# Kernel optimization log

Hardware: AMD Instinct MI355X
Metric: run time of the kernel (lower is better)

The kernel has to match this reference:

```python
import jax, jax.numpy as jnp
import numpy as np

B, L, D = 4096, 200, 64
N_ITEMS, N_USERS, N_RATINGS = 100000, 100000, 5


def setup_inputs() -> dict:
    key = jax.random.key(0)
    ks = jax.random.split(key, 10)
    nodes = jax.random.randint(ks[0], (B,), 0, N_USERS)
    history_uv = jax.random.randint(ks[1], (B, L), 0, N_ITEMS)
    history_r = jax.random.randint(ks[2], (B, L), 0, N_RATINGS)
    s = 1.0 / np.sqrt(D)
    v2e = jax.random.normal(ks[3], (N_ITEMS, D), dtype=jnp.float32)
    r2e = jax.random.normal(ks[4], (N_RATINGS, D), dtype=jnp.float32)
    # torch Linear: weight is [out, in]
    w1_W = jax.random.uniform(ks[5], (D, 2 * D), dtype=jnp.float32, minval=-s, maxval=s)
    w1_b = jax.random.uniform(ks[6], (D,), dtype=jnp.float32, minval=-s, maxval=s)
    w2_W = jax.random.uniform(ks[7], (D, D), dtype=jnp.float32, minval=-s, maxval=s)
    w2_b = jax.random.uniform(ks[8], (D,), dtype=jnp.float32, minval=-s, maxval=s)
    return {
        "v2e": v2e, "r2e": r2e,
        "w1_W": w1_W, "w1_b": w1_b, "w2_W": w2_W, "w2_b": w2_b,
        "nodes": nodes, "history_uv": history_uv, "history_r": history_r,
    }


def reference(v2e, r2e, w1_W, w1_b, w2_W, w2_b, nodes, history_uv, history_r):
    # Gather item and rating embeddings for every (node, history slot): [B, L, D]
    e_uv = v2e[history_uv]
    e_r = r2e[history_r]
    # concat -> [B, L, 2D], two-layer MLP with ReLU
    x = jnp.concatenate([e_uv, e_r], axis=-1)
    h = jax.nn.relu(jnp.einsum("bli,oi->blo", x, w1_W) + w1_b)
    o = jax.nn.relu(jnp.einsum("bli,oi->blo", h, w2_W) + w2_b)
    # uv=True branch: plain mean over the history dimension (nodes/u2e unused)
    return jnp.mean(o, axis=1)  # [B, D]
```

## Files before the change

kernel.cpp:

```cpp
#include <hip/hip_runtime.h>

#define NITEMS 100000
#define NRATE  5
#define BB     4096
#define LL     200
#define DD     64
#define NBUV   391

typedef short short8  __attribute__((ext_vector_type(8)));
typedef short short4v __attribute__((ext_vector_type(4)));
typedef float f32x4   __attribute__((ext_vector_type(4)));

static __device__ __forceinline__ short f2bf(float f) {
  unsigned u = __builtin_bit_cast(unsigned, f);
  u += 0x7fffu + ((u >> 16) & 1u);
  return (short)(u >> 16);
}
static __device__ __forceinline__ float bf2f(short s) {
  return __builtin_bit_cast(float, (unsigned)((unsigned short)s) << 16);
}
static __device__ __forceinline__ int kperm(int p) {
  return ((p & 3) << 4) | (p >> 2);
}

__global__ __launch_bounds__(256) void k_pre(
    const float* __restrict__ v2e, const float* __restrict__ r2e,
    const float* __restrict__ w1W, const float* __restrict__ w1b,
    const float* __restrict__ w2W,
    short* __restrict__ pre_uv, short* __restrict__ w2p,
    float* __restrict__ r5p)
{
  const int tid = threadIdx.x;
  const int blk = blockIdx.x;

  if (blk >= NBUV) {
    for (int idx = tid; idx < 64 * 64; idx += 256) {
      const int o = idx >> 6, p = idx & 63;
      w2p[idx] = f2bf(w2W[o * 64 + kperm(p)]);
    }
    for (int idx = tid; idx < NRATE * 64; idx += 256) {
      const int r = idx >> 6, p = idx & 63;
      const int o = kperm(p);
      const float4* wr = reinterpret_cast<const float4*>(w1W + o * 128 + 64);
      const float4* rr = reinterpret_cast<const float4*>(r2e + r * 64);
      float s = w1b[o];
#pragma unroll
      for (int q = 0; q < 16; ++q) {
        const float4 a = wr[q], b = rr[q];
        s += a.x * b.x + a.y * b.y + a.z * b.z + a.w * b.w;
      }
      r5p[r * 64 + p] = s;
    }
    return;
  }

  const int wave = tid >> 6, lane = tid & 63;
  const int n = lane & 15, quad = lane >> 4;

  short8 bfr[2][4];
#pragma unroll
  for (int nt = 0; nt < 4; ++nt)
#pragma unroll
    for (int kh = 0; kh < 2; ++kh) {
      const float4* p = reinterpret_cast<const float4*>(
          w1W + (nt * 16 + n) * 128 + kh * 32 + quad * 8);
      const float4 x0 = p[0], x1 = p[1];
      short8 f;
      f[0] = f2bf(x0.x); f[1] = f2bf(x0.y); f[2] = f2bf(x0.z); f[3] = f2bf(x0.w);
      f[4] = f2bf(x1.x); f[5] = f2bf(x1.y); f[6] = f2bf(x1.z); f[7] = f2bf(x1.w);
      bfr[kh][nt] = f;
    }

  const int ibase_w = blk * 256 + wave * 64;

  float4 cur0, cur1, cur2, cur3;
  {
    const int row = min(ibase_w + n, NITEMS - 1);
    const float4* p = reinterpret_cast<const float4*>(v2e + (size_t)row * 64 + quad * 8);
    cur0 = p[0]; cur1 = p[1];
    const float4* q = reinterpret_cast<const float4*>(v2e + (size_t)row * 64 + 32 + quad * 8);
    cur2 = q[0]; cur3 = q[1];
  }

#pragma unroll
  for (int it = 0; it < 4; ++it) {
    float4 nx0, nx1, nx2, nx3;
    if (it < 3) {
      const int row = min(ibase_w + (it + 1) * 16 + n, NITEMS - 1);
      const float4* p = reinterpret_cast<const float4*>(v2e + (size_t)row * 64 + quad * 8);
      nx0 = p[0]; nx1 = p[1];
      const float4* q = reinterpret_cast<const float4*>(v2e + (size_t)row * 64 + 32 + quad * 8);
      nx2 = q[0]; nx3 = q[1];
    }

    short8 afr[2];
    {
      short8 a;
      a[0] = f2bf(cur0.x); a[1] = f2bf(cur0.y); a[2] = f2bf(cur0.z); a[3] = f2bf(cur0.w);
      a[4] = f2bf(cur1.x); a[5] = f2bf(cur1.y); a[6] = f2bf(cur1.z); a[7] = f2bf(cur1.w);
      afr[0] = a;
      a[0] = f2bf(cur2.x); a[1] = f2bf(cur2.y); a[2] = f2bf(cur2.z); a[3] = f2bf(cur2.w);
      a[4] = f2bf(cur3.x); a[5] = f2bf(cur3.y); a[6] = f2bf(cur3.z); a[7] = f2bf(cur3.w);
      afr[1] = a;
    }

    f32x4 d[4];
#pragma unroll
    for (int nt = 0; nt < 4; ++nt) {
      f32x4 z = {0.f, 0.f, 0.f, 0.f};
      z = __builtin_amdgcn_mfma_f32_16x16x32_bf16(afr[0], bfr[0][nt], z, 0, 0, 0);
      z = __builtin_amdgcn_mfma_f32_16x16x32_bf16(afr[1], bfr[1][nt], z, 0, 0, 0);
      d[nt] = z;
    }

#pragma unroll
    for (int r = 0; r < 4; ++r) {
      const int item = ibase_w + it * 16 + quad * 4 + r;
      if (item < NITEMS) {
        short4v s = {f2bf(d[0][r]), f2bf(d[1][r]), f2bf(d[2][r]), f2bf(d[3][r])};
        *reinterpret_cast<short4v*>(pre_uv + (size_t)item * 64 + n * 4) = s;
      }
    }

    if (it < 3) { cur0 = nx0; cur1 = nx1; cur2 = nx2; cur3 = nx3; }
  }
}

__global__ __launch_bounds__(256) void k_main(
    const short* __restrict__ pre_uv, const float* __restrict__ r5p,
    const short* __restrict__ w2p, const float* __restrict__ w2b,
    const int* __restrict__ huv, const int* __restrict__ hrr,
    float* __restrict__ out)
{
  __shared__ __align__(16) float s_r5[5 * 68];
  __shared__ float red[4][64];

  const int tid  = threadIdx.x;
  const int wave = tid >> 6, lane = tid & 63;
  const int n = lane & 15, quad = lane >> 4;
  const int b = blockIdx.x;
  const int ntiles = (wave == 0) ? 4 : 3;

  for (int idx = tid; idx < 5 * 64; idx += 256)
    s_r5[(idx >> 6) * 68 + (idx & 63)] = r5p[idx];

  const int* hu = huv + b * LL;
  const int* hr = hrr + b * LL;
  int iv[4] = {0, 0, 0, 0}, ir[4] = {0, 0, 0, 0};
#pragma unroll
  for (int t = 0; t < 4; ++t)
    if (t < ntiles) {
      const int lc = min(wave * 16 + t * 64 + n, LL - 1);
      iv[t] = hu[lc];
      ir[t] = hr[lc];
    }

  short8 bfr[2][4];
#pragma unroll
  for (int nt = 0; nt < 4; ++nt)
#pragma unroll
    for (int kh = 0; kh < 2; ++kh)
      bfr[kh][nt] = *reinterpret_cast<const short8*>(
          w2p + (nt * 16 + n) * 64 + kh * 32 + quad * 8);

  float bias[4];
#pragma unroll
  for (int nt = 0; nt < 4; ++nt) bias[nt] = w2b[nt * 16 + n];

  short8 u[4][2];
#pragma unroll
  for (int t = 0; t < 4; ++t)
    if (t < ntiles)
#pragma unroll
      for (int kh = 0; kh < 2; ++kh)
        u[t][kh] = *reinterpret_cast<const short8*>(
            pre_uv + (size_t)iv[t] * 64 + kh * 32 + quad * 8);

  __syncthreads();

  float acc[4] = {0.f, 0.f, 0.f, 0.f};
#pragma unroll
  for (int t = 0; t < 4; ++t) {
    if (t >= ntiles) continue;
    short8 afr[2];
#pragma unroll
    for (int kh = 0; kh < 2; ++kh) {
      const float4* rp = reinterpret_cast<const float4*>(
          s_r5 + ir[t] * 68 + kh * 32 + quad * 8);
      const float4 r0 = rp[0], r1 = rp[1];
      const float rv[8] = {r0.x, r0.y, r0.z, r0.w, r1.x, r1.y, r1.z, r1.w};
      short8 a;
#pragma unroll
      for (int j = 0; j < 8; ++j) {
        const float h = bf2f(u[t][kh][j]) + rv[j];
        a[j] = f2bf(fmaxf(h, 0.f));
      }
      afr[kh] = a;
    }

    f32x4 d[4];
#pragma unroll
    for (int nt = 0; nt < 4; ++nt) {
      f32x4 z = {0.f, 0.f, 0.f, 0.f};
      z = __builtin_amdgcn_mfma_f32_16x16x32_bf16(afr[0], bfr[0][nt], z, 0, 0, 0);
      z = __builtin_amdgcn_mfma_f32_16x16x32_bf16(afr[1], bfr[1][nt], z, 0, 0, 0);
      d[nt] = z;
    }

    const int lbase = wave * 16 + t * 64;
#pragma unroll
    for (int nt = 0; nt < 4; ++nt)
#pragma unroll
      for (int r = 0; r < 4; ++r) {
        const int rl = lbase + quad * 4 + r;
        const float v = fmaxf(d[nt][r] + bias[nt], 0.f);
        acc[nt] += (rl < LL) ? v : 0.f;
      }
  }

#pragma unroll
  for (int nt = 0; nt < 4; ++nt) {
    float v = acc[nt];
    v += __shfl_xor(v, 16, 64);
    v += __shfl_xor(v, 32, 64);
    acc[nt] = v;
  }

  if (lane < 16) {
#pragma unroll
    for (int nt = 0; nt < 4; ++nt) red[wave][nt * 16 + lane] = acc[nt];
  }
  __syncthreads();
  if (tid < 64) {
    const float s = red[0][tid] + red[1][tid] + red[2][tid] + red[3][tid];
    out[b * 64 + tid] = s * (1.0f / (float)LL);
  }
}

__global__ __launch_bounds__(256) void k_fallback(
    const float* __restrict__ v2e, const float* __restrict__ r2e,
    const float* __restrict__ w1W, const float* __restrict__ w1b,
    const float* __restrict__ w2W, const float* __restrict__ w2b,
    const int* __restrict__ huv, const int* __restrict__ hrr,
    float* __restrict__ out)
{
  __shared__ float sw1[64][129];
  __shared__ float sw2[64][65];
  __shared__ float sx[4][128];
  __shared__ float sh[4][64];
  __shared__ float red[4][64];

  const int tid = threadIdx.x;
  const int wave = tid >> 6, lane = tid & 63;
  const int b = blockIdx.x;

  for (int idx = tid; idx < 64 * 128; idx += 256) sw1[idx >> 7][idx & 127] = w1W[idx];
  for (int idx = tid; idx < 64 * 64; idx += 256) sw2[idx >> 6][idx & 63] = w2W[idx];
  __syncthreads();

  const float b1o = w1b[lane], b2o = w2b[lane];
  float acc = 0.f;

  for (int l = wave; l < LL; l += 4) {
    const int iv = huv[b * LL + l];
    const int ir = hrr[b * LL + l];
    sx[wave][lane]      = v2e[iv * 64 + lane];
    sx[wave][64 + lane] = r2e[ir * 64 + lane];
    __syncthreads();
    float h = b1o;
    for (int i = 0; i < 128; ++i) h += sx[wave][i] * sw1[lane][i];
    sh[wave][lane] = fmaxf(h, 0.f);
    __syncthreads();
    float o = b2o;
    for (int i = 0; i < 64; ++i) o += sh[wave][i] * sw2[lane][i];
    acc += fmaxf(o, 0.f);
  }

  red[wave][lane] = acc;
  __syncthreads();
  if (tid < 64) {
    const float s = red[0][tid] + red[1][tid] + red[2][tid] + red[3][tid];
    out[b * 64 + tid] = s * (1.0f / (float)LL);
  }
}

extern "C" void kernel_launch(void* const* d_in, const int* in_sizes, int n_in,
                              void* d_out, int out_size, void* d_ws, size_t ws_size,
                              hipStream_t stream) {
  (void)in_sizes; (void)n_in; (void)out_size;
  const float* v2e = (const float*)d_in[0];
  const float* r2e = (const float*)d_in[1];
  const float* w1W = (const float*)d_in[2];
  const float* w1b = (const float*)d_in[3];
  const float* w2W = (const float*)d_in[4];
  const float* w2b = (const float*)d_in[5];
  const int* huv = (const int*)d_in[7];
  const int* hrr = (const int*)d_in[8];
  float* out = (float*)d_out;

  const size_t OFF_R5 = (size_t)NITEMS * 64 * sizeof(short);
  const size_t OFF_W2 = OFF_R5 + NRATE * 64 * sizeof(float);
  const size_t NEED   = OFF_W2 + 64 * 64 * sizeof(short);

  if (ws_size >= NEED) {
    short* pre_uv = (short*)d_ws;
    float* r5p    = (float*)((char*)d_ws + OFF_R5);
    short* w2p    = (short*)((char*)d_ws + OFF_W2);

    k_pre<<<NBUV + 1, 256, 0, stream>>>(v2e, r2e, w1W, w1b, w2W, pre_uv, w2p, r5p);
    k_main<<<BB, 256, 0, stream>>>(pre_uv, r5p, w2p, w2b, huv, hrr, out);
  } else {
    k_fallback<<<BB, 256, 0, stream>>>(v2e, r2e, w1W, w1b, w2W, w2b, huv, hrr, out);
  }
}
```

Baseline: 125.0 us.

## Split item precompute across more blocks and vectorize bf16 packing in both kernels

The item-projection kernel now launches four times as many blocks, each wave handling a single 16-item tile instead of looping over four with software prefetch. This aims for more parallelism and memory-level concurrency. bf16 conversion now packs two values with a perm instruction. The main kernel unrolls three full tiles, peels the tail tile for wave 0 with a mask, and uses packed float2 arithmetic for the bias, ReLU and accumulation. The tradeoff is less per-wave latency hiding in the precompute and more code size in the main kernel.

```diff
diff --git a/kernel.cpp b/kernel.cpp
--- a/kernel.cpp
+++ b/kernel.cpp
@@ -5,19 +5,24 @@
 #define BB     4096
 #define LL     200
 #define DD     64
-#define NBUV   391
+#define NBUV   1563
 
 typedef short short8  __attribute__((ext_vector_type(8)));
 typedef short short4v __attribute__((ext_vector_type(4)));
 typedef float f32x4   __attribute__((ext_vector_type(4)));
-
+typedef float f32x2   __attribute__((ext_vector_type(2)));
+typedef int   i32x4   __attribute__((ext_vector_type(4)));
+typedef int   i32x2   __attribute__((ext_vector_type(2)));
+
+static __device__ __forceinline__ unsigned rtne16(float f) {
+  unsigned u = __builtin_bit_cast(unsigned, f);
+  return u + 0x7fffu + ((u >> 16) & 1u);
+}
+static __device__ __forceinline__ unsigned pk2bf(float a, float b) {
+  return __builtin_amdgcn_perm(rtne16(b), rtne16(a), 0x07060302u);
+}
 static __device__ __forceinline__ short f2bf(float f) {
-  unsigned u = __builtin_bit_cast(unsigned, f);
-  u += 0x7fffu + ((u >> 16) & 1u);
-  return (short)(u >> 16);
-}
-static __device__ __forceinline__ float bf2f(short s) {
-  return __builtin_bit_cast(float, (unsigned)((unsigned short)s) << 16);
+  return (short)(rtne16(f) >> 16);
 }
 static __device__ __forceinline__ int kperm(int p) {
   return ((p & 3) << 4) | (p >> 2);
@@ -56,6 +61,7 @@
 
   const int wave = tid >> 6, lane = tid & 63;
   const int n = lane & 15, quad = lane >> 4;
+  const int ibase = blk * 64 + wave * 16;
 
   short8 bfr[2][4];
 #pragma unroll
@@ -65,64 +71,39 @@
       const float4* p = reinterpret_cast<const float4*>(
           w1W + (nt * 16 + n) * 128 + kh * 32 + quad * 8);
       const float4 x0 = p[0], x1 = p[1];
-      short8 f;
-      f[0] = f2bf(x0.x); f[1] = f2bf(x0.y); f[2] = f2bf(x0.z); f[3] = f2bf(x0.w);
-      f[4] = f2bf(x1.x); f[5] = f2bf(x1.y); f[6] = f2bf(x1.z); f[7] = f2bf(x1.w);
-      bfr[kh][nt] = f;
-    }
-
-  const int ibase_w = blk * 256 + wave * 64;
-
-  float4 cur0, cur1, cur2, cur3;
-  {
-    const int row = min(ibase_w + n, NITEMS - 1);
-    const float4* p = reinterpret_cast<const float4*>(v2e + (size_t)row * 64 + quad * 8);
-    cur0 = p[0]; cur1 = p[1];
-    const float4* q = reinterpret_cast<const float4*>(v2e + (size_t)row * 64 + 32 + quad * 8);
-    cur2 = q[0]; cur3 = q[1];
-  }
-
-#pragma unroll
-  for (int it = 0; it < 4; ++it) {
-    float4 nx0, nx1, nx2, nx3;
-    if (it < 3) {
-      const int row = min(ibase_w + (it + 1) * 16 + n, NITEMS - 1);
-      const float4* p = reinterpret_cast<const float4*>(v2e + (size_t)row * 64 + quad * 8);
-      nx0 = p[0]; nx1 = p[1];
-      const float4* q = reinterpret_cast<const float4*>(v2e + (size_t)row * 64 + 32 + quad * 8);
-      nx2 = q[0]; nx3 = q[1];
-    }
-
-    short8 afr[2];
-    {
-      short8 a;
-      a[0] = f2bf(cur0.x); a[1] = f2bf(cur0.y); a[2] = f2bf(cur0.z); a[3] = f2bf(cur0.w);
-      a[4] = f2bf(cur1.x); a[5] = f2bf(cur1.y); a[6] = f2bf(cur1.z); a[7] = f2bf(cur1.w);
-      afr[0] = a;
-      a[0] = f2bf(cur2.x); a[1] = f2bf(cur2.y); a[2] = f2bf(cur2.z); a[3] = f2bf(cur2.w);
-      a[4] = f2bf(cur3.x); a[5] = f2bf(cur3.y); a[6] = f2bf(cur3.z); a[7] = f2bf(cur3.w);
-      afr[1] = a;
-    }
-
-    f32x4 d[4];
-#pragma unroll
-    for (int nt = 0; nt < 4; ++nt) {
-      f32x4 z = {0.f, 0.f, 0.f, 0.f};
-      z = __builtin_amdgcn_mfma_f32_16x16x32_bf16(afr[0], bfr[0][nt], z, 0, 0, 0);
-      z = __builtin_amdgcn_mfma_f32_16x16x32_bf16(afr[1], bfr[1][nt], z, 0, 0, 0);
-      d[nt] = z;
-    }
-
-#pragma unroll
-    for (int r = 0; r < 4; ++r) {
-      const int item = ibase_w + it * 16 + quad * 4 + r;
-      if (item < NITEMS) {
-        short4v s = {f2bf(d[0][r]), f2bf(d[1][r]), f2bf(d[2][r]), f2bf(d[3][r])};
-        *reinterpret_cast<short4v*>(pre_uv + (size_t)item * 64 + n * 4) = s;
-      }
-    }
-
-    if (it < 3) { cur0 = nx0; cur1 = nx1; cur2 = nx2; cur3 = nx3; }
+      i32x4 pk = {(int)pk2bf(x0.x, x0.y), (int)pk2bf(x0.z, x0.w),
+                  (int)pk2bf(x1.x, x1.y), (int)pk2bf(x1.z, x1.w)};
+      bfr[kh][nt] = __builtin_bit_cast(short8, pk);
+    }
+
+  const int arow = min(ibase + n, NITEMS - 1);
+  short8 afr[2];
+#pragma unroll
+  for (int kh = 0; kh < 2; ++kh) {
+    const float4* p = reinterpret_cast<const float4*>(
+        v2e + (size_t)arow * 64 + kh * 32 + quad * 8);
+    const float4 x0 = p[0], x1 = p[1];
+    i32x4 pk = {(int)pk2bf(x0.x, x0.y), (int)pk2bf(x0.z, x0.w),
+                (int)pk2bf(x1.x, x1.y), (int)pk2bf(x1.z, x1.w)};
+    afr[kh] = __builtin_bit_cast(short8, pk);
+  }
+
+  f32x4 d[4];
+#pragma unroll
+  for (int nt = 0; nt < 4; ++nt) {
+    f32x4 z = {0.f, 0.f, 0.f, 0.f};
+    z = __builtin_amdgcn_mfma_f32_16x16x32_bf16(afr[0], bfr[0][nt], z, 0, 0, 0);
+    z = __builtin_amdgcn_mfma_f32_16x16x32_bf16(afr[1], bfr[1][nt], z, 0, 0, 0);
+    d[nt] = z;
+  }
+
+#pragma unroll
+  for (int r = 0; r < 4; ++r) {
+    const int item = ibase + quad * 4 + r;
+    if (item < NITEMS) {
+      i32x2 s = {(int)pk2bf(d[0][r], d[1][r]), (int)pk2bf(d[2][r], d[3][r])};
+      *reinterpret_cast<i32x2*>(pre_uv + (size_t)item * 64 + n * 4) = s;
+    }
   }
 }
 
@@ -139,21 +120,25 @@
   const int wave = tid >> 6, lane = tid & 63;
   const int n = lane & 15, quad = lane >> 4;
   const int b = blockIdx.x;
-  const int ntiles = (wave == 0) ? 4 : 3;
 
   for (int idx = tid; idx < 5 * 64; idx += 256)
     s_r5[(idx >> 6) * 68 + (idx & 63)] = r5p[idx];
 
   const int* hu = huv + b * LL;
   const int* hr = hrr + b * LL;
-  int iv[4] = {0, 0, 0, 0}, ir[4] = {0, 0, 0, 0};
-#pragma unroll
-  for (int t = 0; t < 4; ++t)
-    if (t < ntiles) {
-      const int lc = min(wave * 16 + t * 64 + n, LL - 1);
-      iv[t] = hu[lc];
-      ir[t] = hr[lc];
-    }
+  int iv[4], ir[4];
+#pragma unroll
+  for (int t = 0; t < 3; ++t) {
+    const int lc = wave * 16 + t * 64 + n;
+    iv[t] = hu[lc];
+    ir[t] = hr[lc];
+  }
+  const bool has_tail = (wave == 0);
+  if (has_tail) {
+    const int lc = min(192 + n, LL - 1);
+    iv[3] = hu[lc];
+    ir[3] = hr[lc];
+  }
 
   short8 bfr[2][4];
 #pragma unroll
@@ -163,39 +148,48 @@
       bfr[kh][nt] = *reinterpret_cast<const short8*>(
           w2p + (nt * 16 + n) * 64 + kh * 32 + quad * 8);
 
-  float bias[4];
-#pragma unroll
-  for (int nt = 0; nt < 4; ++nt) bias[nt] = w2b[nt * 16 + n];
+  f32x2 bias2[4];
+#pragma unroll
+  for (int nt = 0; nt < 4; ++nt) {
+    const float bv = w2b[nt * 16 + n];
+    bias2[nt] = f32x2{bv, bv};
+  }
 
   short8 u[4][2];
 #pragma unroll
-  for (int t = 0; t < 4; ++t)
-    if (t < ntiles)
-#pragma unroll
-      for (int kh = 0; kh < 2; ++kh)
-        u[t][kh] = *reinterpret_cast<const short8*>(
-            pre_uv + (size_t)iv[t] * 64 + kh * 32 + quad * 8);
+  for (int t = 0; t < 3; ++t)
+#pragma unroll
+    for (int kh = 0; kh < 2; ++kh)
+      u[t][kh] = *reinterpret_cast<const short8*>(
+          pre_uv + (size_t)iv[t] * 64 + kh * 32 + quad * 8);
+  if (has_tail)
+#pragma unroll
+    for (int kh = 0; kh < 2; ++kh)
+      u[3][kh] = *reinterpret_cast<const short8*>(
+          pre_uv + (size_t)iv[3] * 64 + kh * 32 + quad * 8);
 
   __syncthreads();
 
-  float acc[4] = {0.f, 0.f, 0.f, 0.f};
-#pragma unroll
-  for (int t = 0; t < 4; ++t) {
-    if (t >= ntiles) continue;
+  f32x2 acc2[4] = {{0.f, 0.f}, {0.f, 0.f}, {0.f, 0.f}, {0.f, 0.f}};
+
+#pragma unroll
+  for (int t = 0; t < 3; ++t) {
     short8 afr[2];
 #pragma unroll
     for (int kh = 0; kh < 2; ++kh) {
-      const float4* rp = reinterpret_cast<const float4*>(
+      const i32x4 up = __builtin_bit_cast(i32x4, u[t][kh]);
+      const f32x2* rp = reinterpret_cast<const f32x2*>(
           s_r5 + ir[t] * 68 + kh * 32 + quad * 8);
-      const float4 r0 = rp[0], r1 = rp[1];
-      const float rv[8] = {r0.x, r0.y, r0.z, r0.w, r1.x, r1.y, r1.z, r1.w};
-      short8 a;
-#pragma unroll
-      for (int j = 0; j < 8; ++j) {
-        const float h = bf2f(u[t][kh][j]) + rv[j];
-        a[j] = f2bf(fmaxf(h, 0.f));
+      i32x4 hpk;
+#pragma unroll
+      for (int j = 0; j < 4; ++j) {
+        const unsigned p = (unsigned)up[j];
+        f32x2 uf = {__builtin_bit_cast(float, p << 16),
+                    __builtin_bit_cast(float, p & 0xffff0000u)};
+        f32x2 s = uf + rp[j];
+        hpk[j] = (int)pk2bf(fmaxf(s.x, 0.f), fmaxf(s.y, 0.f));
       }
-      afr[kh] = a;
+      afr[kh] = __builtin_bit_cast(short8, hpk);
     }
 
     f32x4 d[4];
@@ -207,20 +201,61 @@
       d[nt] = z;
     }
 
-    const int lbase = wave * 16 + t * 64;
-#pragma unroll
-    for (int nt = 0; nt < 4; ++nt)
-#pragma unroll
-      for (int r = 0; r < 4; ++r) {
-        const int rl = lbase + quad * 4 + r;
-        const float v = fmaxf(d[nt][r] + bias[nt], 0.f);
-        acc[nt] += (rl < LL) ? v : 0.f;
+#pragma unroll
+    for (int nt = 0; nt < 4; ++nt) {
+      f32x2 p0 = f32x2{d[nt][0], d[nt][1]} + bias2[nt];
+      f32x2 p1 = f32x2{d[nt][2], d[nt][3]} + bias2[nt];
+      p0.x = fmaxf(p0.x, 0.f); p0.y = fmaxf(p0.y, 0.f);
+      p1.x = fmaxf(p1.x, 0.f); p1.y = fmaxf(p1.y, 0.f);
+      acc2[nt] += p0 + p1;
+    }
+  }
+
+  if (has_tail) {
+    const float m = (quad < 2) ? 1.0f : 0.0f;
+    short8 afr[2];
+#pragma unroll
+    for (int kh = 0; kh < 2; ++kh) {
+      const i32x4 up = __builtin_bit_cast(i32x4, u[3][kh]);
+      const f32x2* rp = reinterpret_cast<const f32x2*>(
+          s_r5 + ir[3] * 68 + kh * 32 + quad * 8);
+      i32x4 hpk;
+#pragma unroll
+      for (int j = 0; j < 4; ++j) {
+        const unsigned p = (unsigned)up[j];
+        f32x2 uf = {__builtin_bit_cast(float, p << 16),
+                    __builtin_bit_cast(float, p & 0xffff0000u)};
+        f32x2 s = uf + rp[j];
+        hpk[j] = (int)pk2bf(fmaxf(s.x, 0.f), fmaxf(s.y, 0.f));
       }
-  }
-
+      afr[kh] = __builtin_bit_cast(short8, hpk);
+    }
+
+    f32x4 d[4];
+#pragma unroll
+    for (int nt = 0; nt < 4; ++nt) {
+      f32x4 z = {0.f, 0.f, 0.f, 0.f};
+      z = __builtin_amdgcn_mfma_f32_16x16x32_bf16(afr[0], bfr[0][nt], z, 0, 0, 0);
+      z = __builtin_amdgcn_mfma_f32_16x16x32_bf16(afr[1], bfr[1][nt], z, 0, 0, 0);
+      d[nt] = z;
+    }
+
+#pragma unroll
+    for (int nt = 0; nt < 4; ++nt) {
+      f32x2 p0 = f32x2{d[nt][0], d[nt][1]} + bias2[nt];
+      f32x2 p1 = f32x2{d[nt][2], d[nt][3]} + bias2[nt];
+      p0.x = fmaxf(p0.x, 0.f); p0.y = fmaxf(p0.y, 0.f);
+      p1.x = fmaxf(p1.x, 0.f); p1.y = fmaxf(p1.y, 0.f);
+      const f32x2 s = p0 + p1;
+      acc2[nt].x += s.x * m;
+      acc2[nt].y += s.y * m;
+    }
+  }
+
+  float acc[4];
 #pragma unroll
   for (int nt = 0; nt < 4; ++nt) {
-    float v = acc[nt];
+    float v = acc2[nt].x + acc2[nt].y;
     v += __shfl_xor(v, 16, 64);
     v += __shfl_xor(v, 32, 64);
     acc[nt] = v;
```

New measurement: 134.5 us. +7.6%, slower.

## Assign one wavefront per batch row and pack bf16 conversions

Applied to the files above, without the earlier changes.

k_main now gives each wave a whole batch row, processing 13 history tiles per wave instead of splitting 200 slots over four waves. This removes the shared-memory cross-wave reduction and the second barrier, and issues all 26 embedding gathers up front. The fp32-to-bf16 conversion switches from round-to-nearest-even to a cheaper round-half-up, packed pairwise with v_perm. The layer-1 add/ReLU and bias/accumulate steps use float2 vector math. In exchange, register pressure rises from holding 13 tiles of gathered data, and the rounding behaviour changes slightly.

```diff
diff --git a/kernel.cpp b/kernel.cpp
--- a/kernel.cpp
+++ b/kernel.cpp
@@ -8,16 +8,18 @@
 #define NBUV   391
 
 typedef short short8  __attribute__((ext_vector_type(8)));
-typedef short short4v __attribute__((ext_vector_type(4)));
 typedef float f32x4   __attribute__((ext_vector_type(4)));
+typedef float f32x2   __attribute__((ext_vector_type(2)));
+typedef int   i32x4   __attribute__((ext_vector_type(4)));
+typedef int   i32x2   __attribute__((ext_vector_type(2)));
 
 static __device__ __forceinline__ short f2bf(float f) {
-  unsigned u = __builtin_bit_cast(unsigned, f);
-  u += 0x7fffu + ((u >> 16) & 1u);
-  return (short)(u >> 16);
-}
-static __device__ __forceinline__ float bf2f(short s) {
-  return __builtin_bit_cast(float, (unsigned)((unsigned short)s) << 16);
+  return (short)((__builtin_bit_cast(unsigned, f) + 0x8000u) >> 16);
+}
+static __device__ __forceinline__ unsigned pk2bf(float a, float b) {
+  const unsigned ua = __builtin_bit_cast(unsigned, a) + 0x8000u;
+  const unsigned ub = __builtin_bit_cast(unsigned, b) + 0x8000u;
+  return __builtin_amdgcn_perm(ub, ua, 0x07060302u);
 }
 static __device__ __forceinline__ int kperm(int p) {
   return ((p & 3) << 4) | (p >> 2);
@@ -65,10 +67,9 @@
       const float4* p = reinterpret_cast<const float4*>(
           w1W + (nt * 16 + n) * 128 + kh * 32 + quad * 8);
       const float4 x0 = p[0], x1 = p[1];
-      short8 f;
-      f[0] = f2bf(x0.x); f[1] = f2bf(x0.y); f[2] = f2bf(x0.z); f[3] = f2bf(x0.w);
-      f[4] = f2bf(x1.x); f[5] = f2bf(x1.y); f[6] = f2bf(x1.z); f[7] = f2bf(x1.w);
-      bfr[kh][nt] = f;
+      i32x4 pk = {(int)pk2bf(x0.x, x0.y), (int)pk2bf(x0.z, x0.w),
+                  (int)pk2bf(x1.x, x1.y), (int)pk2bf(x1.z, x1.w)};
+      bfr[kh][nt] = __builtin_bit_cast(short8, pk);
     }
 
   const int ibase_w = blk * 256 + wave * 64;
@@ -95,13 +96,12 @@
 
     short8 afr[2];
     {
-      short8 a;
-      a[0] = f2bf(cur0.x); a[1] = f2bf(cur0.y); a[2] = f2bf(cur0.z); a[3] = f2bf(cur0.w);
-      a[4] = f2bf(cur1.x); a[5] = f2bf(cur1.y); a[6] = f2bf(cur1.z); a[7] = f2bf(cur1.w);
-      afr[0] = a;
-      a[0] = f2bf(cur2.x); a[1] = f2bf(cur2.y); a[2] = f2bf(cur2.z); a[3] = f2bf(cur2.w);
-      a[4] = f2bf(cur3.x); a[5] = f2bf(cur3.y); a[6] = f2bf(cur3.z); a[7] = f2bf(cur3.w);
-      afr[1] = a;
+      i32x4 pk0 = {(int)pk2bf(cur0.x, cur0.y), (int)pk2bf(cur0.z, cur0.w),
+                   (int)pk2bf(cur1.x, cur1.y), (int)pk2bf(cur1.z, cur1.w)};
+      afr[0] = __builtin_bit_cast(short8, pk0);
+      i32x4 pk1 = {(int)pk2bf(cur2.x, cur2.y), (int)pk2bf(cur2.z, cur2.w),
+                   (int)pk2bf(cur3.x, cur3.y), (int)pk2bf(cur3.z, cur3.w)};
+      afr[1] = __builtin_bit_cast(short8, pk1);
     }
 
     f32x4 d[4];
@@ -117,8 +117,8 @@
     for (int r = 0; r < 4; ++r) {
       const int item = ibase_w + it * 16 + quad * 4 + r;
       if (item < NITEMS) {
-        short4v s = {f2bf(d[0][r]), f2bf(d[1][r]), f2bf(d[2][r]), f2bf(d[3][r])};
-        *reinterpret_cast<short4v*>(pre_uv + (size_t)item * 64 + n * 4) = s;
+        i32x2 s = {(int)pk2bf(d[0][r], d[1][r]), (int)pk2bf(d[2][r], d[3][r])};
+        *reinterpret_cast<i32x2*>(pre_uv + (size_t)item * 64 + n * 4) = s;
       }
     }
 
@@ -133,27 +133,37 @@
     float* __restrict__ out)
 {
   __shared__ __align__(16) float s_r5[5 * 68];
-  __shared__ float red[4][64];
 
   const int tid  = threadIdx.x;
   const int wave = tid >> 6, lane = tid & 63;
   const int n = lane & 15, quad = lane >> 4;
-  const int b = blockIdx.x;
-  const int ntiles = (wave == 0) ? 4 : 3;
+  const int b = blockIdx.x * 4 + wave;
 
   for (int idx = tid; idx < 5 * 64; idx += 256)
     s_r5[(idx >> 6) * 68 + (idx & 63)] = r5p[idx];
 
   const int* hu = huv + b * LL;
   const int* hr = hrr + b * LL;
-  int iv[4] = {0, 0, 0, 0}, ir[4] = {0, 0, 0, 0};
-#pragma unroll
-  for (int t = 0; t < 4; ++t)
-    if (t < ntiles) {
-      const int lc = min(wave * 16 + t * 64 + n, LL - 1);
-      iv[t] = hu[lc];
-      ir[t] = hr[lc];
-    }
+
+  int iv[13], ir[13];
+#pragma unroll
+  for (int t = 0; t < 12; ++t) {
+    iv[t] = hu[t * 16 + n];
+    ir[t] = hr[t * 16 + n];
+  }
+  {
+    const int lc = min(192 + n, LL - 1);
+    iv[12] = hu[lc];
+    ir[12] = hr[lc];
+  }
+
+  short8 u[13][2];
+#pragma unroll
+  for (int t = 0; t < 13; ++t)
+#pragma unroll
+    for (int kh = 0; kh < 2; ++kh)
+      u[t][kh] = *reinterpret_cast<const short8*>(
+          pre_uv + (size_t)iv[t] * 64 + kh * 32 + quad * 8);
 
   short8 bfr[2][4];
 #pragma unroll
@@ -163,39 +173,36 @@
       bfr[kh][nt] = *reinterpret_cast<const short8*>(
           w2p + (nt * 16 + n) * 64 + kh * 32 + quad * 8);
 
-  float bias[4];
-#pragma unroll
-  for (int nt = 0; nt < 4; ++nt) bias[nt] = w2b[nt * 16 + n];
-
-  short8 u[4][2];
-#pragma unroll
-  for (int t = 0; t < 4; ++t)
-    if (t < ntiles)
-#pragma unroll
-      for (int kh = 0; kh < 2; ++kh)
-        u[t][kh] = *reinterpret_cast<const short8*>(
-            pre_uv + (size_t)iv[t] * 64 + kh * 32 + quad * 8);
+  f32x2 bias2[4];
+#pragma unroll
+  for (int nt = 0; nt < 4; ++nt) {
+    const float bv = w2b[nt * 16 + n];
+    bias2[nt] = f32x2{bv, bv};
+  }
 
   __syncthreads();
 
-  float acc[4] = {0.f, 0.f, 0.f, 0.f};
-#pragma unroll
-  for (int t = 0; t < 4; ++t) {
-    if (t >= ntiles) continue;
+  const float tailm = (quad < 2) ? 1.0f : 0.0f;
+  f32x2 acc2[4] = {{0.f, 0.f}, {0.f, 0.f}, {0.f, 0.f}, {0.f, 0.f}};
+
+#pragma unroll
+  for (int t = 0; t < 13; ++t) {
     short8 afr[2];
 #pragma unroll
     for (int kh = 0; kh < 2; ++kh) {
-      const float4* rp = reinterpret_cast<const float4*>(
+      const i32x4 up = __builtin_bit_cast(i32x4, u[t][kh]);
+      const f32x2* rp = reinterpret_cast<const f32x2*>(
           s_r5 + ir[t] * 68 + kh * 32 + quad * 8);
-      const float4 r0 = rp[0], r1 = rp[1];
-      const float rv[8] = {r0.x, r0.y, r0.z, r0.w, r1.x, r1.y, r1.z, r1.w};
-      short8 a;
-#pragma unroll
-      for (int j = 0; j < 8; ++j) {
-        const float h = bf2f(u[t][kh][j]) + rv[j];
-        a[j] = f2bf(fmaxf(h, 0.f));
+      i32x4 hpk;
+#pragma unroll
+      for (int j = 0; j < 4; ++j) {
+        const unsigned p = (unsigned)up[j];
+        f32x2 uf = {__builtin_bit_cast(float, p << 16),
+                    __builtin_bit_cast(float, p & 0xffff0000u)};
+        const f32x2 s = uf + rp[j];
+        hpk[j] = (int)pk2bf(fmaxf(s.x, 0.f), fmaxf(s.y, 0.f));
       }
-      afr[kh] = a;
+      afr[kh] = __builtin_bit_cast(short8, hpk);
     }
 
     f32x4 d[4];
@@ -207,34 +214,28 @@
       d[nt] = z;
     }
 
-    const int lbase = wave * 16 + t * 64;
-#pragma unroll
-    for (int nt = 0; nt < 4; ++nt)
-#pragma unroll
-      for (int r = 0; r < 4; ++r) {
-        const int rl = lbase + quad * 4 + r;
-        const float v = fmaxf(d[nt][r] + bias[nt], 0.f);
-        acc[nt] += (rl < LL) ? v : 0.f;
-      }
-  }
-
+#pragma unroll
+    for (int nt = 0; nt < 4; ++nt) {
+      f32x2 p0 = f32x2{d[nt][0], d[nt][1]} + bias2[nt];
+      f32x2 p1 = f32x2{d[nt][2], d[nt][3]} + bias2[nt];
+      p0.x = fmaxf(p0.x, 0.f); p0.y = fmaxf(p0.y, 0.f);
+      p1.x = fmaxf(p1.x, 0.f); p1.y = fmaxf(p1.y, 0.f);
+      f32x2 s = p0 + p1;
+      if (t == 12) { s.x *= tailm; s.y *= tailm; }
+      acc2[nt] += s;
+    }
+  }
+
+  float acc[4];
 #pragma unroll
   for (int nt = 0; nt < 4; ++nt) {
-    float v = acc[nt];
+    float v = acc2[nt].x + acc2[nt].y;
     v += __shfl_xor(v, 16, 64);
     v += __shfl_xor(v, 32, 64);
     acc[nt] = v;
   }
 
-  if (lane < 16) {
-#pragma unroll
-    for (int nt = 0; nt < 4; ++nt) red[wave][nt * 16 + lane] = acc[nt];
-  }
-  __syncthreads();
-  if (tid < 64) {
-    const float s = red[0][tid] + red[1][tid] + red[2][tid] + red[3][tid];
-    out[b * 64 + tid] = s * (1.0f / (float)LL);
-  }
+  out[b * 64 + quad * 16 + n] = acc[quad] * (1.0f / (float)LL);
 }
 
 __global__ __launch_bounds__(256) void k_fallback(
@@ -308,7 +309,7 @@
     short* w2p    = (short*)((char*)d_ws + OFF_W2);
 
     k_pre<<<NBUV + 1, 256, 0, stream>>>(v2e, r2e, w1W, w1b, w2W, pre_uv, w2p, r5p);
-    k_main<<<BB, 256, 0, stream>>>(pre_uv, r5p, w2p, w2b, huv, hrr, out);
+    k_main<<<BB / 4, 256, 0, stream>>>(pre_uv, r5p, w2p, w2b, huv, hrr, out);
   } else {
     k_fallback<<<BB, 256, 0, stream>>>(v2e, r2e, w1W, w1b, w2W, w2b, huv, hrr, out);
   }
```

After: 115.7 us. 1.08x faster.
